# Performance work log

Hardware: AMD Instinct MI355X
Metric: run time of the kernel (lower is better)

## Reference

```python
import jax, jax.numpy as jnp
import numpy as np

STAGE = 100
EPS = 1e-5


def bin_affine(w, shift_aff, sign_aff):
    """Vectorized equivalent of the 100-iteration range-mask loop.
    Original: for i in range(stage): mask = (w >= lo_i) & (w < hi_i);
              shift += w.detach()*shift_aff[i]*mask; sign += w.detach()*sign_aff[i]*mask.
    Equivalent to bucketize + gather + scale. Element equal to w.max() falls
    outside every half-open bin (strict <), so it gets zero, matching torch.
    w is detached in the original, so gradients flow only to the affines.
    """
    wf = w.reshape(-1)
    wmin, wmax = wf.min(), wf.max()
    t = (wf - wmin) / (wmax - wmin) * STAGE
    idx = jnp.floor(t).astype(jnp.int32)
    valid = (idx >= 0) & (idx < STAGE)
    idxc = jnp.clip(idx, 0, STAGE - 1)
    wd = jax.lax.stop_gradient(wf)
    shift = jnp.where(valid, wd * shift_aff[idxc], 0.0)
    sign = jnp.where(valid, wd * sign_aff[idxc], 0.0)
    return shift.reshape(w.shape), sign.reshape(w.shape)


def eff_weight(w, shift_aff, sign_aff):
    # Conv2dShift forward with externally-assigned continuous shift/sign:
    # effective weight = sign * 2**shift (deepshift-style, unrounded).
    shift, sign = bin_affine(w, shift_aff, sign_aff)
    return sign * jnp.exp2(shift)


def conv2d(x, w, stride=1, pad=0, groups=1):
    return jax.lax.conv_general_dilated(
        x, w, (stride, stride), [(pad, pad), (pad, pad)],
        dimension_numbers=("NCHW", "OIHW", "NCHW"), feature_group_count=groups)


def batchnorm(x, g, b):
    m = x.mean((0, 2, 3), keepdims=True)
    v = x.var((0, 2, 3), keepdims=True)
    return (x - m) * jax.lax.rsqrt(v + EPS) * g[None, :, None, None] + b[None, :, None, None]


def setup_inputs() -> dict:
    key = jax.random.key(0)
    ks = jax.random.split(key, 16)
    d = {
        "x": jax.random.normal(ks[0], (32, 256, 56, 56), jnp.float32),
        "w_ds": 0.05 * jax.random.normal(ks[1], (512, 256, 1, 1), jnp.float32),
        "w_c1": 0.05 * jax.random.normal(ks[2], (128, 256, 1, 1), jnp.float32),
        "w_peg": 0.05 * jax.random.normal(ks[3], (128, 1, 3, 3), jnp.float32),
        "w_c2": 0.05 * jax.random.normal(ks[4], (128, 128, 3, 3), jnp.float32),
        "w_c3": 0.05 * jax.random.normal(ks[5], (512, 128, 1, 1), jnp.float32),
        "aff_ds_shift": jax.random.normal(ks[6], (STAGE,), jnp.float32),
        "aff_ds_sign": jax.random.normal(ks[7], (STAGE,), jnp.float32),
        "aff_c1_shift": jax.random.normal(ks[8], (STAGE,), jnp.float32),
        "aff_c1_sign": jax.random.normal(ks[9], (STAGE,), jnp.float32),
        "aff_c2_shift": jax.random.normal(ks[10], (STAGE,), jnp.float32),
        "aff_c2_sign": jax.random.normal(ks[11], (STAGE,), jnp.float32),
        "aff_c3_shift": jax.random.normal(ks[12], (STAGE,), jnp.float32),
        "aff_c3_sign": jax.random.normal(ks[13], (STAGE,), jnp.float32),
        "g_bn_ds": jnp.ones((512,), jnp.float32),
        "b_bn_ds": jnp.zeros((512,), jnp.float32),
        "g_bn1": jnp.ones((128,), jnp.float32),
        "b_bn1": jnp.zeros((128,), jnp.float32),
        "g_bn2": jnp.ones((128,), jnp.float32),
        "b_bn2": jnp.zeros((128,), jnp.float32),
        "g_bn3": jnp.ones((512,), jnp.float32),
        "b_bn3": jnp.zeros((512,), jnp.float32),
    }
    return d


def reference(x, w_ds, w_c1, w_peg, w_c2, w_c3,
              aff_ds_shift, aff_ds_sign, aff_c1_shift, aff_c1_sign,
              aff_c2_shift, aff_c2_sign, aff_c3_shift, aff_c3_sign,
              g_bn_ds, b_bn_ds, g_bn1, b_bn1, g_bn2, b_bn2, g_bn3, b_bn3):
    # main branch (fmap_size == self.fmap_size): bin downsample + conv1/2/3 weights
    wds_e = eff_weight(w_ds, aff_ds_shift, aff_ds_sign)
    wc1_e = eff_weight(w_c1, aff_c1_shift, aff_c1_sign)
    wc2_e = eff_weight(w_c2, aff_c2_shift, aff_c2_sign)
    wc3_e = eff_weight(w_c3, aff_c3_shift, aff_c3_sign)

    # downsample = Conv1x1 -> BN -> ReLU
    residual = jax.nn.relu(batchnorm(conv2d(x, wds_e), g_bn_ds, b_bn_ds))

    h = conv2d(x, wc1_e)                                   # 1x1, 256->128
    h = conv2d(h, w_peg, stride=1, pad=1, groups=128)      # PEG depthwise 3x3
    h = jax.nn.relu(batchnorm(h, g_bn1, b_bn1))            # bn1 + act1
    h = conv2d(h, wc2_e, stride=1, pad=1)                  # 3x3, 128->128
    h = jax.nn.relu(batchnorm(h, g_bn2, b_bn2))            # bn2 + act2
    h = conv2d(h, wc3_e)                                   # 1x1, 128->512
    h = batchnorm(h, g_bn3, b_bn3)                         # bn3
    return jax.nn.relu(h + residual)                       # act3
```

## Files before the change

kernel.cpp:

```cpp
#include <hip/hip_runtime.h>
#include <stdint.h>


#define HW    3136
#define WID   56
#define NB    32
#define FLIP_TENSOR 1

#define OFF_MM    0
#define OFF_SC1   8
#define OFF_BI1   136
#define OFF_SC2   264
#define OFF_BI2   392
#define OFF_SC3   520
#define OFF_BI3   1032
#define OFF_SCDS  1544
#define OFF_BIDS  2056
#define WB_BASE_BYTES 16384ULL
#define WB_M  0ULL
#define WB_C2 163840ULL
#define WB_C3 311296ULL
#define PS1S_B  786432ULL
#define PS1Q_B  802816ULL
#define PS2S_B  819200ULL
#define PS2Q_B  1622016ULL
#define PS3S_B  2424832ULL
#define PS3Q_B  5636096ULL
#define PSDS_B  8847360ULL
#define PSDQ_B  12058624ULL
#define AC_BASE_BYTES 16777216ULL
#define AC_A 0ULL
#define AC_B 12845056ULL
#define AC_C 25690112ULL
#define AC_R 77070336ULL
#define NSLOT 1568

typedef __attribute__((ext_vector_type(8))) short bfrag8;
typedef __attribute__((ext_vector_type(4))) float facc4;

__device__ __forceinline__ unsigned short f2bf(float f) {
  unsigned u = __float_as_uint(f);
  u = u + 0x7FFFu + ((u >> 16) & 1u);
  return (unsigned short)(u >> 16);
}
__device__ __forceinline__ float bf2f(unsigned short h) {
  return __uint_as_float(((unsigned)h) << 16);
}
__device__ __forceinline__ unsigned fmap(float f) {
  unsigned u = __float_as_uint(f);
  return (u & 0x80000000u) ? ~u : (u | 0x80000000u);
}
__device__ __forceinline__ float funmap(unsigned m) {
  unsigned u = (m & 0x80000000u) ? (m & 0x7FFFFFFFu) : ~m;
  return __uint_as_float(u);
}

__global__ void k_mm_init(unsigned* mm) {
  int t = threadIdx.x;
  if (t < 4) { mm[2 * t] = 0xFFFFFFFFu; mm[2 * t + 1] = 0u; }
}

__device__ __forceinline__ void tensor_of(int g0, int& tensor, int& local0) {
  if (g0 < 131072)      { tensor = 0; local0 = g0; }
  else if (g0 < 163840) { tensor = 1; local0 = g0 - 131072; }
  else if (g0 < 311296) { tensor = 2; local0 = g0 - 163840; }
  else                  { tensor = 3; local0 = g0 - 311296; }
}

__global__ __launch_bounds__(256) void k_minmax(
    const float* __restrict__ w_ds, const float* __restrict__ w_c1,
    const float* __restrict__ w_c2, const float* __restrict__ w_c3,
    unsigned* __restrict__ mm) {
  __shared__ unsigned smin[256], smax[256];
  int t = threadIdx.x;
  int tensor, local0;
  tensor_of(blockIdx.x * 1024, tensor, local0);
  const float* src = (tensor == 0) ? w_ds : (tensor == 1) ? w_c1 : (tensor == 2) ? w_c2 : w_c3;
  float4 v = *(const float4*)(src + local0 + t * 4);
  unsigned mn, mx;
  {
    unsigned m0 = fmap(v.x), m1 = fmap(v.y), m2 = fmap(v.z), m3 = fmap(v.w);
    mn = min(min(m0, m1), min(m2, m3));
    mx = max(max(m0, m1), max(m2, m3));
  }
  smin[t] = mn; smax[t] = mx;
  __syncthreads();
  for (int s = 128; s > 0; s >>= 1) {
    if (t < s) { smin[t] = min(smin[t], smin[t + s]); smax[t] = max(smax[t], smax[t + s]); }
    __syncthreads();
  }
  if (t == 0) {
    atomicMin(&mm[2 * tensor], smin[0]);
    atomicMax(&mm[2 * tensor + 1], smax[0]);
  }
}

__global__ __launch_bounds__(256) void k_effw(
    const float* __restrict__ w_ds, const float* __restrict__ w_c1,
    const float* __restrict__ w_c2, const float* __restrict__ w_c3,
    const float* __restrict__ sh_ds, const float* __restrict__ sg_ds,
    const float* __restrict__ sh_c1, const float* __restrict__ sg_c1,
    const float* __restrict__ sh_c2, const float* __restrict__ sg_c2,
    const float* __restrict__ sh_c3, const float* __restrict__ sg_c3,
    const unsigned* __restrict__ mm, unsigned short* __restrict__ wb) {
  int t = threadIdx.x;
  int tensor, local0;
  tensor_of(blockIdx.x * 1024, tensor, local0);
  const float* src = (tensor == 0) ? w_ds : (tensor == 1) ? w_c1 : (tensor == 2) ? w_c2 : w_c3;
  const float* sha = (tensor == 0) ? sh_ds : (tensor == 1) ? sh_c1 : (tensor == 2) ? sh_c2 : sh_c3;
  const float* sga = (tensor == 0) ? sg_ds : (tensor == 1) ? sg_c1 : (tensor == 2) ? sg_c2 : sg_c3;
  float wmin = funmap(mm[2 * tensor]);
  float wmax = funmap(mm[2 * tensor + 1]);
  float rng = __fsub_rn(wmax, wmin);
  float I32 = __fdiv_rn(rng, 100.0f);
  float edge100 = __fadd_rn(wmin, __fmul_rn(100.0f, I32));
  bool s32 = (wmax < edge100);
  bool binmax = (tensor == FLIP_TENSOR) ? !s32 : s32;
  float4 v4 = *(const float4*)(src + local0 + t * 4);
  float vs[4] = {v4.x, v4.y, v4.z, v4.w};
#pragma unroll
  for (int e = 0; e < 4; ++e) {
    int l = local0 + t * 4 + e;
    float v = vs[e];
    float ew;
    if (v == wmax) {
      ew = binmax ? (v * sga[99]) * exp2f(v * sha[99]) : 0.0f;
    } else {
      float tt = __fmul_rn(__fdiv_rn(__fsub_rn(v, wmin), rng), 100.0f);
      int idx = (int)floorf(tt);
      bool valid = (idx >= 0) && (idx < 100);
      int ic = valid ? idx : 0;
      float shift = valid ? v * sha[ic] : 0.0f;
      float sign  = valid ? v * sga[ic] : 0.0f;
      ew = sign * exp2f(shift);
    }
    unsigned short h = f2bf(ew);
    if (tensor == 0) {
      int co = l >> 8, ci = l & 255;
      wb[WB_M + (size_t)(128 + co) * 256 + ci] = h;
    } else if (tensor == 1) {
      int co = l >> 8, ci = l & 255;
      wb[WB_M + (size_t)co * 256 + ci] = h;
    } else if (tensor == 2) {
      int co = l / 1152; int r2 = l - co * 1152;
      int ci = r2 / 9; int tap = r2 - ci * 9;
      wb[WB_C2 + (size_t)co * 1152 + tap * 128 + ci] = h;
    } else {
      int co = l >> 7, ci = l & 127;
      wb[WB_C3 + (size_t)co * 128 + ci] = h;
    }
  }
}

template <int CI, int TAPS, int KBLK, int COOUT, bool XBF,
          bool FUSEIN, bool STATS, bool MERGED, int NCOB>
__global__ __launch_bounds__(256) void k_mconv6(
    const void* __restrict__ Xv, const unsigned short* __restrict__ Wt,
    unsigned short* __restrict__ Y1, unsigned short* __restrict__ Y2,
    const float* __restrict__ fsc, const float* __restrict__ fbi,
    float* __restrict__ PS, float* __restrict__ PQ) {
  constexpr int NSP = (TAPS == 9) ? 192 : 64;
  constexpr int ST  = KBLK + 2;
  __shared__ short lx[NSP][ST];
  __shared__ float redS[128][2], redQ[128][2];
  const int tid  = threadIdx.x;
  const int lane = tid & 63;
  const int wv   = tid >> 6;
  int lid = blockIdx.x;
  int xcd = lid & 7;
  int j   = lid >> 3;
  int co_blk = j % NCOB;
  int t_  = xcd * 196 + j / NCOB;
  int sp_blk = t_ % 49;
  int n      = t_ / 49;
  const int s0  = sp_blk * 64;
  const int co0 = co_blk * 128;
  const int NK  = CI * TAPS;
  const unsigned short* Xh = (const unsigned short*)Xv + (size_t)n * CI * HW;
  const float*          Xf = (const float*)Xv + (size_t)n * CI * HW;

  const int wco  = (wv >> 1) * 64;
  const int wsp  = (wv & 1) * 32;
  const int lrow = lane & 15;
  const int lkg  = lane >> 4;
  const int kb8  = lkg * 8;

  int spl[2], yc[2], xc[2];
#pragma unroll
  for (int nn = 0; nn < 2; ++nn) {
    spl[nn] = wsp + nn * 16 + lrow;
    int s = s0 + spl[nn];
    yc[nn] = s / WID;
    xc[nn] = s - yc[nn] * WID;
  }

  facc4 acc[4][2];
#pragma unroll
  for (int m = 0; m < 4; ++m)
#pragma unroll
    for (int nn = 0; nn < 2; ++nn) acc[m][nn] = (facc4)(0.0f);

  for (int k0 = 0; k0 < CI; k0 += KBLK) {
    __syncthreads();
    if (TAPS == 9) {
#pragma unroll
      for (int i = 0; i < 3; ++i) {
        int task = tid + i * 256;
        int spi = task % 192;
        int kc  = task / 192;
        int p = s0 - 64 + spi;
        short v[8];
        if ((unsigned)p < (unsigned)HW) {
          const unsigned short* pp = Xh + (size_t)(k0 + kc * 8) * HW + p;
#pragma unroll
          for (int jj = 0; jj < 8; ++jj) {
            if (FUSEIN) {
              float f = bf2f(pp[(size_t)jj * HW]);
              f = fmaxf(fmaf(f, fsc[k0 + kc * 8 + jj], fbi[k0 + kc * 8 + jj]), 0.0f);
              v[jj] = (short)f2bf(f);
            } else {
              v[jj] = (short)pp[(size_t)jj * HW];
            }
          }
        } else {
#pragma unroll
          for (int jj = 0; jj < 8; ++jj) v[jj] = 0;
        }
        *(short4*)(&lx[spi][kc * 8])     = (short4){v[0], v[1], v[2], v[3]};
        *(short4*)(&lx[spi][kc * 8 + 4]) = (short4){v[4], v[5], v[6], v[7]};
      }
    } else {
#pragma unroll
      for (int i = 0; i < KBLK / 32; ++i) {
        int task = tid + i * 256;
        int spi = task & 63;
        int kc  = task >> 6;
        int p = s0 + spi;
        short v[8];
        if (XBF) {
          const unsigned short* pp = Xh + (size_t)(k0 + kc * 8) * HW + p;
#pragma unroll
          for (int jj = 0; jj < 8; ++jj) {
            if (FUSEIN) {
              float f = bf2f(pp[(size_t)jj * HW]);
              f = fmaxf(fmaf(f, fsc[k0 + kc * 8 + jj], fbi[k0 + kc * 8 + jj]), 0.0f);
              v[jj] = (short)f2bf(f);
            } else {
              v[jj] = (short)pp[(size_t)jj * HW];
            }
          }
        } else {
          const float* pf = Xf + (size_t)(k0 + kc * 8) * HW + p;
#pragma unroll
          for (int jj = 0; jj < 8; ++jj) v[jj] = (short)f2bf(pf[(size_t)jj * HW]);
        }
        *(short4*)(&lx[spi][kc * 8])     = (short4){v[0], v[1], v[2], v[3]};
        *(short4*)(&lx[spi][kc * 8 + 4]) = (short4){v[4], v[5], v[6], v[7]};
      }
    }
    __syncthreads();
    if (TAPS == 1) {
      bfrag8 af[KBLK / 32][4];
#pragma unroll
      for (int kk = 0; kk < KBLK / 32; ++kk)
#pragma unroll
        for (int m = 0; m < 4; ++m)
          af[kk][m] = *(const bfrag8*)(Wt +
              (size_t)(co0 + wco + m * 16 + lrow) * NK + k0 + kk * 32 + kb8);
#pragma unroll
      for (int kk = 0; kk < KBLK / 32; ++kk) {
#pragma unroll
        for (int nn = 0; nn < 2; ++nn) {
          bfrag8 b = *(const bfrag8*)(&lx[spl[nn]][kk * 32 + kb8]);
#pragma unroll
          for (int m = 0; m < 4; ++m)
            acc[m][nn] = __builtin_amdgcn_mfma_f32_16x16x32_bf16(
                af[kk][m], b, acc[m][nn], 0, 0, 0);
        }
      }
    } else {
      bfrag8 afc[4], afn[4];
#pragma unroll
      for (int m = 0; m < 4; ++m)
        afc[m] = *(const bfrag8*)(Wt +
            (size_t)(co0 + wco + m * 16 + lrow) * NK + k0 + kb8);
      for (int tap = 0; tap < 9; ++tap) {
        if (tap < 8) {
#pragma unroll
          for (int m = 0; m < 4; ++m)
            afn[m] = *(const bfrag8*)(Wt +
                (size_t)(co0 + wco + m * 16 + lrow) * NK + (tap + 1) * CI + k0 + kb8);
        }
        const int dy = tap / 3 - 1;
        const int dx = tap % 3 - 1;
        const int off = dy * WID + dx;
#pragma unroll
        for (int nn = 0; nn < 2; ++nn) {
          bfrag8 b = *(const bfrag8*)(&lx[64 + spl[nn] + off][kb8]);
          bool valid = ((unsigned)(xc[nn] + dx) < (unsigned)WID) &&
                       ((unsigned)(yc[nn] + dy) < (unsigned)WID);
          if (!valid) b = (bfrag8)(short)0;
#pragma unroll
          for (int m = 0; m < 4; ++m)
            acc[m][nn] = __builtin_amdgcn_mfma_f32_16x16x32_bf16(
                afc[m], b, acc[m][nn], 0, 0, 0);
        }
#pragma unroll
        for (int m = 0; m < 4; ++m) afc[m] = afn[m];
      }
    }
  }
  unsigned short* Yb;
  int coL, COst;
  if (MERGED) {
    if (co0 < 128) { Yb = Y1; coL = co0; COst = 128; }
    else           { Yb = Y2; coL = co0 - 128; COst = 512; }
  } else {
    Yb = Y1; coL = co0; COst = COOUT;
  }
#pragma unroll
  for (int m = 0; m < 4; ++m)
#pragma unroll
    for (int nn = 0; nn < 2; ++nn)
#pragma unroll
      for (int r = 0; r < 4; ++r) {
        int co_g = coL + wco + m * 16 + lkg * 4 + r;
        int sp_g = s0 + wsp + nn * 16 + lrow;
        Yb[((size_t)n * COst + co_g) * HW + sp_g] = f2bf(acc[m][nn][r]);
      }
  const bool do_st = STATS && (!MERGED || co0 >= 128);
  if (do_st) {
#pragma unroll
    for (int m = 0; m < 4; ++m)
#pragma unroll
      for (int r = 0; r < 4; ++r) {
        float sv = acc[m][0][r] + acc[m][1][r];
        float qv = acc[m][0][r] * acc[m][0][r] + acc[m][1][r] * acc[m][1][r];
#pragma unroll
        for (int d = 1; d < 16; d <<= 1) {
          sv += __shfl_xor(sv, d);
          qv += __shfl_xor(qv, d);
        }
        if (lrow == 0) {
          int col = wco + m * 16 + lkg * 4 + r;
          redS[col][wv & 1] = sv;
          redQ[col][wv & 1] = qv;
        }
      }
    __syncthreads();
    if (tid < 128) {
      int cstat = (MERGED ? co0 - 128 : co0) + tid;
      int slot = n * 49 + sp_blk;
      PS[(size_t)cstat * NSLOT + slot] = redS[tid][0] + redS[tid][1];
      PQ[(size_t)cstat * NSLOT + slot] = redQ[tid][0] + redQ[tid][1];
    }
  }
}

__global__ __launch_bounds__(256) void k_dw(
    const unsigned short* __restrict__ Xin, const float* __restrict__ wp,
    unsigned short* __restrict__ Yout,
    float* __restrict__ PS, float* __restrict__ PQ) {
  __shared__ float pl[HW];
  __shared__ float rs[256], rq[256];
  int bid = blockIdx.x;
  int c = bid & 127;
  int n = bid >> 7;
  const unsigned short* src = Xin + (size_t)bid * HW;
  int t = threadIdx.x;
  for (int q = t; q < HW / 4; q += 256) {
    ushort4 h4 = *(const ushort4*)(src + q * 4);
    pl[q * 4 + 0] = bf2f(h4.x); pl[q * 4 + 1] = bf2f(h4.y);
    pl[q * 4 + 2] = bf2f(h4.z); pl[q * 4 + 3] = bf2f(h4.w);
  }
  float w[9];
#pragma unroll
  for (int k = 0; k < 9; ++k) w[k] = wp[c * 9 + k];
  __syncthreads();
  unsigned short* dst = Yout + (size_t)bid * HW;
  float accS = 0.0f, accQ = 0.0f;
  for (int q = t; q < HW / 4; q += 256) {
    float o[4];
#pragma unroll
    for (int e = 0; e < 4; ++e) {
      int s = q * 4 + e;
      int y = s / WID, xcc = s - y * WID;
      float accv = 0.0f;
#pragma unroll
      for (int ky = 0; ky < 3; ++ky) {
        int yy = y + ky - 1;
        if (yy < 0 || yy >= WID) continue;
#pragma unroll
        for (int kx = 0; kx < 3; ++kx) {
          int xx = xcc + kx - 1;
          if (xx < 0 || xx >= WID) continue;
          accv = fmaf(w[ky * 3 + kx], pl[yy * WID + xx], accv);
        }
      }
      o[e] = accv;
      accS += accv;
      accQ = fmaf(accv, accv, accQ);
    }
    ushort4 ov;
    ov.x = f2bf(o[0]); ov.y = f2bf(o[1]); ov.z = f2bf(o[2]); ov.w = f2bf(o[3]);
    *(ushort4*)(dst + q * 4) = ov;
  }
  rs[t] = accS; rq[t] = accQ;
  __syncthreads();
  for (int st = 128; st > 0; st >>= 1) {
    if (t < st) { rs[t] += rs[t + st]; rq[t] += rq[t + st]; }
    __syncthreads();
  }
  if (t == 0) {
    PS[(size_t)c * NB + n] = rs[0];
    PQ[(size_t)c * NB + n] = rq[0];
  }
}

__global__ __launch_bounds__(256) void k_red(
    const float* __restrict__ S, const float* __restrict__ Q,
    const float* __restrict__ g, const float* __restrict__ b,
    float* __restrict__ sc_o, float* __restrict__ bi_o, int npart) {
  int c = blockIdx.x, t = threadIdx.x;
  double s = 0.0, q = 0.0;
  for (int i = t; i < npart; i += 256) {
    s += S[(size_t)c * npart + i];
    q += Q[(size_t)c * npart + i];
  }
  __shared__ double ss[256], qq[256];
  ss[t] = s; qq[t] = q;
  __syncthreads();
  for (int st = 128; st > 0; st >>= 1) {
    if (t < st) { ss[t] += ss[t + st]; qq[t] += qq[t + st]; }
    __syncthreads();
  }
  if (t == 0) {
    double nn = (double)HW * NB;
    double mean = ss[0] / nn;
    double var = qq[0] / nn - mean * mean;
    float rstd = (float)(1.0 / sqrt(var + 1e-5));
    float sc = g[c] * rstd;
    sc_o[c] = sc;
    bi_o[c] = b[c] - (float)mean * sc;
  }
}

__global__ __launch_bounds__(256) void k_final(
    float* __restrict__ out, const unsigned short* __restrict__ hC,
    const unsigned short* __restrict__ r,
    const float* __restrict__ sc3, const float* __restrict__ bi3,
    const float* __restrict__ scds, const float* __restrict__ bids) {
  const int QPN = 512 * 784;
  const int total = NB * QPN;
  for (int q = blockIdx.x * 256 + threadIdx.x; q < total; q += gridDim.x * 256) {
    int qn = q % QPN;
    int c = qn / 784;
    ushort4 hh = *(const ushort4*)(hC + (size_t)q * 4);
    ushort4 rh = *(const ushort4*)(r + (size_t)q * 4);
    float s3 = sc3[c], b3 = bi3[c], sd = scds[c], bd = bids[c];
    float4 o;
    float rb;
    rb = fmaxf(fmaf(bf2f(rh.x), sd, bd), 0.0f); o.x = fmaxf(fmaf(bf2f(hh.x), s3, b3) + rb, 0.0f);
    rb = fmaxf(fmaf(bf2f(rh.y), sd, bd), 0.0f); o.y = fmaxf(fmaf(bf2f(hh.y), s3, b3) + rb, 0.0f);
    rb = fmaxf(fmaf(bf2f(rh.z), sd, bd), 0.0f); o.z = fmaxf(fmaf(bf2f(hh.z), s3, b3) + rb, 0.0f);
    rb = fmaxf(fmaf(bf2f(rh.w), sd, bd), 0.0f); o.w = fmaxf(fmaf(bf2f(hh.w), s3, b3) + rb, 0.0f);
    *(float4*)(out + (size_t)q * 4) = o;
  }
}

extern "C" void kernel_launch(void* const* d_in, const int* in_sizes, int n_in,
                              void* d_out, int out_size, void* d_ws, size_t ws_size,
                              hipStream_t stream) {
  const float *x = nullptr, *w_ds = nullptr, *w_c1 = nullptr, *w_peg = nullptr,
              *w_c2 = nullptr, *w_c3 = nullptr;
  const float* aff[8] = {nullptr};
  const float* v512[4] = {nullptr};
  const float* v128[4] = {nullptr};
  int naff = 0, n512 = 0, n128 = 0;
  for (int i = 0; i < n_in; ++i) {
    const float* p = (const float*)d_in[i];
    switch (in_sizes[i]) {
      case 25690112: x = p; break;
      case 131072:   w_ds = p; break;
      case 32768:    w_c1 = p; break;
      case 1152:     w_peg = p; break;
      case 147456:   w_c2 = p; break;
      case 65536:    w_c3 = p; break;
      case 100:      if (naff < 8) aff[naff++] = p; break;
      case 512:      if (n512 < 4) v512[n512++] = p; break;
      case 128:      if (n128 < 4) v128[n128++] = p; break;
      default: break;
    }
  }
  const float *a_ds_sh = aff[0], *a_ds_sg = aff[1], *a_c1_sh = aff[2], *a_c1_sg = aff[3];
  const float *a_c2_sh = aff[4], *a_c2_sg = aff[5], *a_c3_sh = aff[6], *a_c3_sg = aff[7];
  const float *g_ds = v512[0], *b_ds = v512[1], *g3 = v512[2], *b3 = v512[3];
  const float *g1 = v128[0], *b1 = v128[1], *g2 = v128[2], *b2 = v128[3];

  float* ws  = (float*)d_ws;
  float* out = (float*)d_out;
  unsigned* mm = (unsigned*)(ws + OFF_MM);
  unsigned short* wb = (unsigned short*)((char*)d_ws + WB_BASE_BYTES);
  unsigned short* ac = (unsigned short*)((char*)d_ws + AC_BASE_BYTES);
  unsigned short* bufA = ac + AC_A;
  unsigned short* bufB = ac + AC_B;
  unsigned short* bufC = ac + AC_C;
  unsigned short* bufR = ac + AC_R;
  float* ps1S = (float*)((char*)d_ws + PS1S_B);
  float* ps1Q = (float*)((char*)d_ws + PS1Q_B);
  float* ps2S = (float*)((char*)d_ws + PS2S_B);
  float* ps2Q = (float*)((char*)d_ws + PS2Q_B);
  float* ps3S = (float*)((char*)d_ws + PS3S_B);
  float* ps3Q = (float*)((char*)d_ws + PS3Q_B);
  float* psdS = (float*)((char*)d_ws + PSDS_B);
  float* psdQ = (float*)((char*)d_ws + PSDQ_B);

  k_mm_init<<<dim3(1), dim3(64), 0, stream>>>(mm);
  k_minmax<<<dim3(368), dim3(256), 0, stream>>>(w_ds, w_c1, w_c2, w_c3, mm);
  k_effw<<<dim3(368), dim3(256), 0, stream>>>(
      w_ds, w_c1, w_c2, w_c3,
      a_ds_sh, a_ds_sg, a_c1_sh, a_c1_sg, a_c2_sh, a_c2_sg, a_c3_sh, a_c3_sg,
      mm, wb);

  k_mconv6<256, 1, 128, 0, false, false, true, true, 5>
      <<<dim3(7840), dim3(256), 0, stream>>>(
      x, wb + WB_M, bufA, bufR, nullptr, nullptr, psdS, psdQ);
  k_red<<<dim3(512), dim3(256), 0, stream>>>(psdS, psdQ, g_ds, b_ds,
                                             ws + OFF_SCDS, ws + OFF_BIDS, NSLOT);
  k_dw<<<dim3(NB * 128), dim3(256), 0, stream>>>(bufA, w_peg, bufB, ps1S, ps1Q);
  k_red<<<dim3(128), dim3(256), 0, stream>>>(ps1S, ps1Q, g1, b1,
                                             ws + OFF_SC1, ws + OFF_BI1, NB);
  k_mconv6<128, 9, 32, 128, true, true, true, false, 1>
      <<<dim3(1568), dim3(256), 0, stream>>>(
      bufB, wb + WB_C2, bufA, nullptr, ws + OFF_SC1, ws + OFF_BI1, ps2S, ps2Q);
  k_red<<<dim3(128), dim3(256), 0, stream>>>(ps2S, ps2Q, g2, b2,
                                             ws + OFF_SC2, ws + OFF_BI2, NSLOT);
  k_mconv6<128, 1, 128, 512, true, true, true, false, 4>
      <<<dim3(6272), dim3(256), 0, stream>>>(
      bufA, wb + WB_C3, bufC, nullptr, ws + OFF_SC2, ws + OFF_BI2, ps3S, ps3Q);
  k_red<<<dim3(512), dim3(256), 0, stream>>>(ps3S, ps3Q, g3, b3,
                                             ws + OFF_SC3, ws + OFF_BI3, NSLOT);
  k_final<<<dim3(4096), dim3(256), 0, stream>>>(out, bufC, bufR,
                                                ws + OFF_SC3, ws + OFF_BI3,
                                                ws + OFF_SCDS, ws + OFF_BIDS);
}
```

Before: 545.4 us.

## Switch intermediate activations to channels-last layout with input transpose kernel

Adds a transpose kernel that converts x to bf16 NHWC, and switches the conv and depthwise kernels to read and write channels-last intermediates with 16-byte vector loads instead of strided per-channel gathers. The depthwise kernel is re-tiled over spatial blocks with per-slot BN statistics. The final conv writes fp32 directly into the output buffer, and the epilogue then updates it in place, which drops the bf16 intermediate buffer. In exchange it adds an extra pass over x and moves more fp32 traffic through the last conv.

```diff
diff --git a/kernel.cpp b/kernel.cpp
--- a/kernel.cpp
+++ b/kernel.cpp
@@ -21,18 +21,18 @@
 #define WB_C2 163840ULL
 #define WB_C3 311296ULL
 #define PS1S_B  786432ULL
-#define PS1Q_B  802816ULL
-#define PS2S_B  819200ULL
-#define PS2Q_B  1622016ULL
-#define PS3S_B  2424832ULL
-#define PS3Q_B  5636096ULL
-#define PSDS_B  8847360ULL
-#define PSDQ_B  12058624ULL
-#define AC_BASE_BYTES 16777216ULL
-#define AC_A 0ULL
-#define AC_B 12845056ULL
-#define AC_C 25690112ULL
-#define AC_R 77070336ULL
+#define PS1Q_B  1589248ULL
+#define PS2S_B  2392064ULL
+#define PS2Q_B  3194880ULL
+#define PS3S_B  3997696ULL
+#define PS3Q_B  7208960ULL
+#define PSDS_B  10420224ULL
+#define PSDQ_B  13631488ULL
+#define AC_BASE_BYTES 33554432ULL
+#define AC_XT 0ULL
+#define AC_A  25690112ULL
+#define AC_B  38535168ULL
+#define AC_R  51380224ULL
 #define NSLOT 1568
 
 typedef __attribute__((ext_vector_type(8))) short bfrag8;
@@ -152,16 +152,45 @@
   }
 }
 
-template <int CI, int TAPS, int KBLK, int COOUT, bool XBF,
-          bool FUSEIN, bool STATS, bool MERGED, int NCOB>
-__global__ __launch_bounds__(256) void k_mconv6(
-    const void* __restrict__ Xv, const unsigned short* __restrict__ Wt,
+__global__ __launch_bounds__(256) void k_tr(
+    const float* __restrict__ x, unsigned short* __restrict__ XT) {
+  __shared__ short lt[64 * 258];
+  int bid = blockIdx.x;
+  int sp_blk = bid % 49, n = bid / 49;
+  int s0 = sp_blk * 64;
+  int t = threadIdx.x;
+  {
+    const float* row = x + ((size_t)n * 256 + t) * HW + s0;
+#pragma unroll
+    for (int i = 0; i < 16; ++i) {
+      float4 v = *(const float4*)(row + i * 4);
+      lt[(i * 4 + 0) * 258 + t] = (short)f2bf(v.x);
+      lt[(i * 4 + 1) * 258 + t] = (short)f2bf(v.y);
+      lt[(i * 4 + 2) * 258 + t] = (short)f2bf(v.z);
+      lt[(i * 4 + 3) * 258 + t] = (short)f2bf(v.w);
+    }
+  }
+  __syncthreads();
+  {
+    int spi = t >> 2, cb = (t & 3) * 64;
+    unsigned short* dst = XT + ((size_t)n * HW + s0 + spi) * 256 + cb;
+    const short* srcl = &lt[spi * 258 + cb];
+#pragma unroll
+    for (int q = 0; q < 8; ++q)
+      *(float4*)((short*)dst + q * 8) = *(const float4*)(srcl + q * 8);
+  }
+}
+
+template <int CIN, int TAPS, int KBLK, int NCOB, bool FUSEIN, bool STATS, int MODE>
+__global__ __launch_bounds__(256) void k_mconv7(
+    const unsigned short* __restrict__ Xn, const unsigned short* __restrict__ Wt,
     unsigned short* __restrict__ Y1, unsigned short* __restrict__ Y2,
+    float* __restrict__ Yf,
     const float* __restrict__ fsc, const float* __restrict__ fbi,
     float* __restrict__ PS, float* __restrict__ PQ) {
   constexpr int NSP = (TAPS == 9) ? 192 : 64;
   constexpr int ST  = KBLK + 2;
-  __shared__ short lx[NSP][ST];
+  __shared__ short lx[NSP * ST];
   __shared__ float redS[128][2], redQ[128][2];
   const int tid  = threadIdx.x;
   const int lane = tid & 63;
@@ -175,9 +204,8 @@
   int n      = t_ / 49;
   const int s0  = sp_blk * 64;
   const int co0 = co_blk * 128;
-  const int NK  = CI * TAPS;
-  const unsigned short* Xh = (const unsigned short*)Xv + (size_t)n * CI * HW;
-  const float*          Xf = (const float*)Xv + (size_t)n * CI * HW;
+  const int NK  = CIN * TAPS;
+  const size_t nsp0 = (size_t)n * HW + s0;
 
   const int wco  = (wv >> 1) * 64;
   const int wsp  = (wv & 1) * 32;
@@ -200,62 +228,51 @@
 #pragma unroll
     for (int nn = 0; nn < 2; ++nn) acc[m][nn] = (facc4)(0.0f);
 
-  for (int k0 = 0; k0 < CI; k0 += KBLK) {
+  for (int k0 = 0; k0 < CIN; k0 += KBLK) {
     __syncthreads();
     if (TAPS == 9) {
 #pragma unroll
       for (int i = 0; i < 3; ++i) {
         int task = tid + i * 256;
-        int spi = task % 192;
-        int kc  = task / 192;
+        int spi = task >> 2, ch = (task & 3) * 8;
         int p = s0 - 64 + spi;
-        short v[8];
+        unsigned short vv[8];
         if ((unsigned)p < (unsigned)HW) {
-          const unsigned short* pp = Xh + (size_t)(k0 + kc * 8) * HW + p;
-#pragma unroll
-          for (int jj = 0; jj < 8; ++jj) {
+          float4 raw = *(const float4*)(Xn + ((size_t)n * HW + p) * CIN + k0 + ch);
+          const unsigned short* pv = (const unsigned short*)&raw;
+#pragma unroll
+          for (int q = 0; q < 8; ++q) {
             if (FUSEIN) {
-              float f = bf2f(pp[(size_t)jj * HW]);
-              f = fmaxf(fmaf(f, fsc[k0 + kc * 8 + jj], fbi[k0 + kc * 8 + jj]), 0.0f);
-              v[jj] = (short)f2bf(f);
-            } else {
-              v[jj] = (short)pp[(size_t)jj * HW];
-            }
+              float f = bf2f(pv[q]);
+              f = fmaxf(fmaf(f, fsc[k0 + ch + q], fbi[k0 + ch + q]), 0.0f);
+              vv[q] = f2bf(f);
+            } else vv[q] = pv[q];
           }
         } else {
 #pragma unroll
-          for (int jj = 0; jj < 8; ++jj) v[jj] = 0;
-        }
-        *(short4*)(&lx[spi][kc * 8])     = (short4){v[0], v[1], v[2], v[3]};
-        *(short4*)(&lx[spi][kc * 8 + 4]) = (short4){v[4], v[5], v[6], v[7]};
+          for (int q = 0; q < 8; ++q) vv[q] = 0;
+        }
+        *(float4*)(&lx[spi * ST + ch]) = *(const float4*)vv;
       }
     } else {
-#pragma unroll
-      for (int i = 0; i < KBLK / 32; ++i) {
-        int task = tid + i * 256;
-        int spi = task & 63;
-        int kc  = task >> 6;
-        int p = s0 + spi;
-        short v[8];
-        if (XBF) {
-          const unsigned short* pp = Xh + (size_t)(k0 + kc * 8) * HW + p;
-#pragma unroll
-          for (int jj = 0; jj < 8; ++jj) {
-            if (FUSEIN) {
-              float f = bf2f(pp[(size_t)jj * HW]);
-              f = fmaxf(fmaf(f, fsc[k0 + kc * 8 + jj], fbi[k0 + kc * 8 + jj]), 0.0f);
-              v[jj] = (short)f2bf(f);
-            } else {
-              v[jj] = (short)pp[(size_t)jj * HW];
-            }
+      int row = tid >> 2, cb = (tid & 3) * 32;
+      const unsigned short* src = Xn + (nsp0 + row) * CIN + k0 + cb;
+#pragma unroll
+      for (int q = 0; q < 4; ++q) {
+        float4 raw = *(const float4*)(src + q * 8);
+        if (FUSEIN) {
+          const unsigned short* pv = (const unsigned short*)&raw;
+          unsigned short vv[8];
+#pragma unroll
+          for (int e = 0; e < 8; ++e) {
+            float f = bf2f(pv[e]);
+            f = fmaxf(fmaf(f, fsc[k0 + cb + q * 8 + e], fbi[k0 + cb + q * 8 + e]), 0.0f);
+            vv[e] = f2bf(f);
           }
+          *(float4*)(&lx[row * ST + cb + q * 8]) = *(const float4*)vv;
         } else {
-          const float* pf = Xf + (size_t)(k0 + kc * 8) * HW + p;
-#pragma unroll
-          for (int jj = 0; jj < 8; ++jj) v[jj] = (short)f2bf(pf[(size_t)jj * HW]);
-        }
-        *(short4*)(&lx[spi][kc * 8])     = (short4){v[0], v[1], v[2], v[3]};
-        *(short4*)(&lx[spi][kc * 8 + 4]) = (short4){v[4], v[5], v[6], v[7]};
+          *(float4*)(&lx[row * ST + cb + q * 8]) = raw;
+        }
       }
     }
     __syncthreads();
@@ -271,7 +288,7 @@
       for (int kk = 0; kk < KBLK / 32; ++kk) {
 #pragma unroll
         for (int nn = 0; nn < 2; ++nn) {
-          bfrag8 b = *(const bfrag8*)(&lx[spl[nn]][kk * 32 + kb8]);
+          bfrag8 b = *(const bfrag8*)(&lx[spl[nn] * ST + kk * 32 + kb8]);
 #pragma unroll
           for (int m = 0; m < 4; ++m)
             acc[m][nn] = __builtin_amdgcn_mfma_f32_16x16x32_bf16(
@@ -289,14 +306,14 @@
 #pragma unroll
           for (int m = 0; m < 4; ++m)
             afn[m] = *(const bfrag8*)(Wt +
-                (size_t)(co0 + wco + m * 16 + lrow) * NK + (tap + 1) * CI + k0 + kb8);
+                (size_t)(co0 + wco + m * 16 + lrow) * NK + (tap + 1) * CIN + k0 + kb8);
         }
         const int dy = tap / 3 - 1;
         const int dx = tap % 3 - 1;
         const int off = dy * WID + dx;
 #pragma unroll
         for (int nn = 0; nn < 2; ++nn) {
-          bfrag8 b = *(const bfrag8*)(&lx[64 + spl[nn] + off][kb8]);
+          bfrag8 b = *(const bfrag8*)(&lx[(64 + spl[nn] + off) * ST + kb8]);
           bool valid = ((unsigned)(xc[nn] + dx) < (unsigned)WID) &&
                        ((unsigned)(yc[nn] + dy) < (unsigned)WID);
           if (!valid) b = (bfrag8)(short)0;
@@ -310,25 +327,40 @@
       }
     }
   }
-  unsigned short* Yb;
-  int coL, COst;
-  if (MERGED) {
-    if (co0 < 128) { Yb = Y1; coL = co0; COst = 128; }
-    else           { Yb = Y2; coL = co0 - 128; COst = 512; }
+  if (MODE == 0 || (MODE == 2 && co0 < 128)) {
+#pragma unroll
+    for (int m = 0; m < 4; ++m)
+#pragma unroll
+      for (int nn = 0; nn < 2; ++nn) {
+        unsigned short o[4];
+#pragma unroll
+        for (int r = 0; r < 4; ++r) o[r] = f2bf(acc[m][nn][r]);
+        size_t addr = (nsp0 + spl[nn]) * 128 + co0 + wco + m * 16 + lkg * 4;
+        *(ushort4*)(Y1 + addr) = *(const ushort4*)o;
+      }
+  } else if (MODE == 2) {
+    int coL = co0 - 128;
+#pragma unroll
+    for (int m = 0; m < 4; ++m)
+#pragma unroll
+      for (int nn = 0; nn < 2; ++nn)
+#pragma unroll
+        for (int r = 0; r < 4; ++r) {
+          int co_g = coL + wco + m * 16 + lkg * 4 + r;
+          Y2[((size_t)n * 512 + co_g) * HW + s0 + spl[nn]] = f2bf(acc[m][nn][r]);
+        }
   } else {
-    Yb = Y1; coL = co0; COst = COOUT;
-  }
-#pragma unroll
-  for (int m = 0; m < 4; ++m)
-#pragma unroll
-    for (int nn = 0; nn < 2; ++nn)
-#pragma unroll
-      for (int r = 0; r < 4; ++r) {
-        int co_g = coL + wco + m * 16 + lkg * 4 + r;
-        int sp_g = s0 + wsp + nn * 16 + lrow;
-        Yb[((size_t)n * COst + co_g) * HW + sp_g] = f2bf(acc[m][nn][r]);
-      }
-  const bool do_st = STATS && (!MERGED || co0 >= 128);
+#pragma unroll
+    for (int m = 0; m < 4; ++m)
+#pragma unroll
+      for (int nn = 0; nn < 2; ++nn)
+#pragma unroll
+        for (int r = 0; r < 4; ++r) {
+          int co_g = co0 + wco + m * 16 + lkg * 4 + r;
+          Yf[((size_t)n * 512 + co_g) * HW + s0 + spl[nn]] = acc[m][nn][r];
+        }
+  }
+  const bool do_st = STATS && (MODE != 2 || co0 >= 128);
   if (do_st) {
 #pragma unroll
     for (int m = 0; m < 4; ++m)
@@ -349,7 +381,7 @@
       }
     __syncthreads();
     if (tid < 128) {
-      int cstat = (MERGED ? co0 - 128 : co0) + tid;
+      int cstat = ((MODE == 2) ? co0 - 128 : co0) + tid;
       int slot = n * 49 + sp_blk;
       PS[(size_t)cstat * NSLOT + slot] = redS[tid][0] + redS[tid][1];
       PQ[(size_t)cstat * NSLOT + slot] = redQ[tid][0] + redQ[tid][1];
@@ -358,62 +390,68 @@
 }
 
 __global__ __launch_bounds__(256) void k_dw(
-    const unsigned short* __restrict__ Xin, const float* __restrict__ wp,
-    unsigned short* __restrict__ Yout,
+    const unsigned short* __restrict__ Ain, const float* __restrict__ wp,
+    unsigned short* __restrict__ Bout,
     float* __restrict__ PS, float* __restrict__ PQ) {
-  __shared__ float pl[HW];
-  __shared__ float rs[256], rq[256];
+  __shared__ float wl[9][128];
+  __shared__ float sS[16][128], sQ[16][128];
   int bid = blockIdx.x;
-  int c = bid & 127;
-  int n = bid >> 7;
-  const unsigned short* src = Xin + (size_t)bid * HW;
+  int sp_blk = bid % 49, n = bid / 49;
+  int s0 = sp_blk * 64;
   int t = threadIdx.x;
-  for (int q = t; q < HW / 4; q += 256) {
-    ushort4 h4 = *(const ushort4*)(src + q * 4);
-    pl[q * 4 + 0] = bf2f(h4.x); pl[q * 4 + 1] = bf2f(h4.y);
-    pl[q * 4 + 2] = bf2f(h4.z); pl[q * 4 + 3] = bf2f(h4.w);
-  }
-  float w[9];
-#pragma unroll
-  for (int k = 0; k < 9; ++k) w[k] = wp[c * 9 + k];
+  if (t < 128) {
+#pragma unroll
+    for (int tap = 0; tap < 9; ++tap) wl[tap][t] = wp[t * 9 + tap];
+  }
   __syncthreads();
-  unsigned short* dst = Yout + (size_t)bid * HW;
-  float accS = 0.0f, accQ = 0.0f;
-  for (int q = t; q < HW / 4; q += 256) {
-    float o[4];
-#pragma unroll
-    for (int e = 0; e < 4; ++e) {
-      int s = q * 4 + e;
-      int y = s / WID, xcc = s - y * WID;
-      float accv = 0.0f;
-#pragma unroll
-      for (int ky = 0; ky < 3; ++ky) {
-        int yy = y + ky - 1;
-        if (yy < 0 || yy >= WID) continue;
-#pragma unroll
-        for (int kx = 0; kx < 3; ++kx) {
-          int xx = xcc + kx - 1;
-          if (xx < 0 || xx >= WID) continue;
-          accv = fmaf(w[ky * 3 + kx], pl[yy * WID + xx], accv);
-        }
-      }
-      o[e] = accv;
-      accS += accv;
-      accQ = fmaf(accv, accv, accQ);
-    }
-    ushort4 ov;
-    ov.x = f2bf(o[0]); ov.y = f2bf(o[1]); ov.z = f2bf(o[2]); ov.w = f2bf(o[3]);
-    *(ushort4*)(dst + q * 4) = ov;
-  }
-  rs[t] = accS; rq[t] = accQ;
+  const int c8 = (t & 15) * 8;
+  const int g  = t >> 4;
+  float wreg[9][8];
+#pragma unroll
+  for (int tap = 0; tap < 9; ++tap)
+#pragma unroll
+    for (int jj = 0; jj < 8; ++jj) wreg[tap][jj] = wl[tap][c8 + jj];
+  float aS[8], aQ[8];
+#pragma unroll
+  for (int jj = 0; jj < 8; ++jj) { aS[jj] = 0.0f; aQ[jj] = 0.0f; }
+  const size_t nb = (size_t)n * HW;
+#pragma unroll
+  for (int it = 0; it < 4; ++it) {
+    int s = s0 + it * 16 + g;
+    int y = s / WID, xx0 = s - y * WID;
+    float accv[8];
+#pragma unroll
+    for (int jj = 0; jj < 8; ++jj) accv[jj] = 0.0f;
+#pragma unroll
+    for (int tap = 0; tap < 9; ++tap) {
+      int dy = tap / 3 - 1, dx = tap % 3 - 1;
+      if ((unsigned)(y + dy) < (unsigned)WID && (unsigned)(xx0 + dx) < (unsigned)WID) {
+        float4 raw = *(const float4*)(Ain + (nb + s + dy * WID + dx) * 128 + c8);
+        const unsigned short* pv = (const unsigned short*)&raw;
+#pragma unroll
+        for (int jj = 0; jj < 8; ++jj)
+          accv[jj] = fmaf(wreg[tap][jj], bf2f(pv[jj]), accv[jj]);
+      }
+    }
+    unsigned short ov[8];
+#pragma unroll
+    for (int jj = 0; jj < 8; ++jj) {
+      ov[jj] = f2bf(accv[jj]);
+      aS[jj] += accv[jj];
+      aQ[jj] = fmaf(accv[jj], accv[jj], aQ[jj]);
+    }
+    *(float4*)(Bout + (nb + s) * 128 + c8) = *(const float4*)ov;
+  }
+#pragma unroll
+  for (int jj = 0; jj < 8; ++jj) { sS[g][c8 + jj] = aS[jj]; sQ[g][c8 + jj] = aQ[jj]; }
   __syncthreads();
-  for (int st = 128; st > 0; st >>= 1) {
-    if (t < st) { rs[t] += rs[t + st]; rq[t] += rq[t + st]; }
-    __syncthreads();
-  }
-  if (t == 0) {
-    PS[(size_t)c * NB + n] = rs[0];
-    PQ[(size_t)c * NB + n] = rq[0];
+  if (t < 128) {
+    float s = 0.0f, q = 0.0f;
+#pragma unroll
+    for (int g2 = 0; g2 < 16; ++g2) { s += sS[g2][t]; q += sQ[g2][t]; }
+    int slot = n * 49 + sp_blk;
+    PS[(size_t)t * NSLOT + slot] = s;
+    PQ[(size_t)t * NSLOT + slot] = q;
   }
 }
 
@@ -446,8 +484,7 @@
 }
 
 __global__ __launch_bounds__(256) void k_final(
-    float* __restrict__ out, const unsigned short* __restrict__ hC,
-    const unsigned short* __restrict__ r,
+    float* __restrict__ out, const unsigned short* __restrict__ r,
     const float* __restrict__ sc3, const float* __restrict__ bi3,
     const float* __restrict__ scds, const float* __restrict__ bids) {
   const int QPN = 512 * 784;
@@ -455,15 +492,15 @@
   for (int q = blockIdx.x * 256 + threadIdx.x; q < total; q += gridDim.x * 256) {
     int qn = q % QPN;
     int c = qn / 784;
-    ushort4 hh = *(const ushort4*)(hC + (size_t)q * 4);
+    float4 h = *(const float4*)(out + (size_t)q * 4);
     ushort4 rh = *(const ushort4*)(r + (size_t)q * 4);
     float s3 = sc3[c], b3 = bi3[c], sd = scds[c], bd = bids[c];
     float4 o;
     float rb;
-    rb = fmaxf(fmaf(bf2f(rh.x), sd, bd), 0.0f); o.x = fmaxf(fmaf(bf2f(hh.x), s3, b3) + rb, 0.0f);
-    rb = fmaxf(fmaf(bf2f(rh.y), sd, bd), 0.0f); o.y = fmaxf(fmaf(bf2f(hh.y), s3, b3) + rb, 0.0f);
-    rb = fmaxf(fmaf(bf2f(rh.z), sd, bd), 0.0f); o.z = fmaxf(fmaf(bf2f(hh.z), s3, b3) + rb, 0.0f);
-    rb = fmaxf(fmaf(bf2f(rh.w), sd, bd), 0.0f); o.w = fmaxf(fmaf(bf2f(hh.w), s3, b3) + rb, 0.0f);
+    rb = fmaxf(fmaf(bf2f(rh.x), sd, bd), 0.0f); o.x = fmaxf(fmaf(h.x, s3, b3) + rb, 0.0f);
+    rb = fmaxf(fmaf(bf2f(rh.y), sd, bd), 0.0f); o.y = fmaxf(fmaf(h.y, s3, b3) + rb, 0.0f);
+    rb = fmaxf(fmaf(bf2f(rh.z), sd, bd), 0.0f); o.z = fmaxf(fmaf(h.z, s3, b3) + rb, 0.0f);
+    rb = fmaxf(fmaf(bf2f(rh.w), sd, bd), 0.0f); o.w = fmaxf(fmaf(h.w, s3, b3) + rb, 0.0f);
     *(float4*)(out + (size_t)q * 4) = o;
   }
 }
@@ -502,10 +539,10 @@
   unsigned* mm = (unsigned*)(ws + OFF_MM);
   unsigned short* wb = (unsigned short*)((char*)d_ws + WB_BASE_BYTES);
   unsigned short* ac = (unsigned short*)((char*)d_ws + AC_BASE_BYTES);
-  unsigned short* bufA = ac + AC_A;
-  unsigned short* bufB = ac + AC_B;
-  unsigned short* bufC = ac + AC_C;
-  unsigned short* bufR = ac + AC_R;
+  unsigned short* bufXT = ac + AC_XT;
+  unsigned short* bufA  = ac + AC_A;
+  unsigned short* bufB  = ac + AC_B;
+  unsigned short* bufR  = ac + AC_R;
   float* ps1S = (float*)((char*)d_ws + PS1S_B);
   float* ps1Q = (float*)((char*)d_ws + PS1Q_B);
   float* ps2S = (float*)((char*)d_ws + PS2S_B);
@@ -521,26 +558,29 @@
       w_ds, w_c1, w_c2, w_c3,
       a_ds_sh, a_ds_sg, a_c1_sh, a_c1_sg, a_c2_sh, a_c2_sg, a_c3_sh, a_c3_sg,
       mm, wb);
-
-  k_mconv6<256, 1, 128, 0, false, false, true, true, 5>
+  k_tr<<<dim3(1568), dim3(256), 0, stream>>>(x, bufXT);
+
+  k_mconv7<256, 1, 128, 5, false, true, 2>
       <<<dim3(7840), dim3(256), 0, stream>>>(
-      x, wb + WB_M, bufA, bufR, nullptr, nullptr, psdS, psdQ);
+      bufXT, wb + WB_M, bufA, bufR, nullptr, nullptr, nullptr, psdS, psdQ);
   k_red<<<dim3(512), dim3(256), 0, stream>>>(psdS, psdQ, g_ds, b_ds,
                                              ws + OFF_SCDS, ws + OFF_BIDS, NSLOT);
-  k_dw<<<dim3(NB * 128), dim3(256), 0, stream>>>(bufA, w_peg, bufB, ps1S, ps1Q);
+  k_dw<<<dim3(1568), dim3(256), 0, stream>>>(bufA, w_peg, bufB, ps1S, ps1Q);
   k_red<<<dim3(128), dim3(256), 0, stream>>>(ps1S, ps1Q, g1, b1,
-                                             ws + OFF_SC1, ws + OFF_BI1, NB);
-  k_mconv6<128, 9, 32, 128, true, true, true, false, 1>
+                                             ws + OFF_SC1, ws + OFF_BI1, NSLOT);
+  k_mconv7<128, 9, 32, 1, true, true, 0>
       <<<dim3(1568), dim3(256), 0, stream>>>(
-      bufB, wb + WB_C2, bufA, nullptr, ws + OFF_SC1, ws + OFF_BI1, ps2S, ps2Q);
+      bufB, wb + WB_C2, bufA, nullptr, nullptr, ws + OFF_SC1, ws + OFF_BI1,
+      ps2S, ps2Q);
   k_red<<<dim3(128), dim3(256), 0, stream>>>(ps2S, ps2Q, g2, b2,
                                              ws + OFF_SC2, ws + OFF_BI2, NSLOT);
-  k_mconv6<128, 1, 128, 512, true, true, true, false, 4>
+  k_mconv7<128, 1, 128, 4, true, true, 3>
       <<<dim3(6272), dim3(256), 0, stream>>>(
-      bufA, wb + WB_C3, bufC, nullptr, ws + OFF_SC2, ws + OFF_BI2, ps3S, ps3Q);
+      bufA, wb + WB_C3, nullptr, nullptr, out, ws + OFF_SC2, ws + OFF_BI2,
+      ps3S, ps3Q);
   k_red<<<dim3(512), dim3(256), 0, stream>>>(ps3S, ps3Q, g3, b3,
                                              ws + OFF_SC3, ws + OFF_BI3, NSLOT);
-  k_final<<<dim3(4096), dim3(256), 0, stream>>>(out, bufC, bufR,
+  k_final<<<dim3(4096), dim3(256), 0, stream>>>(out, bufR,
                                                 ws + OFF_SC3, ws + OFF_BI3,
                                                 ws + OFF_SCDS, ws + OFF_BIDS);
 }
```

New measurement: 601.1 us. 1.1x slower.

## Pre-transpose input to bf16 NHWC and use LDS-direct loads for merged 1x1 conv

Applied to the files above, without the earlier changes.

Adds a transpose kernel that converts the fp32 NCHW input into a bf16 spatial-major (channels-last) buffer. A new specialized merged conv1/downsample kernel then stages this buffer straight into LDS with global_load_lds and an XOR swizzle to avoid bank conflicts. The aim is to cut the fp32 read and in-kernel conversion and transpose cost that the five channel-block passes over x previously repeated. The extra pass writes and re-reads a bf16 copy of x, and that copy reuses buffer C, which is only safe because conv3 writes C later.

```diff
diff --git a/kernel.cpp b/kernel.cpp
--- a/kernel.cpp
+++ b/kernel.cpp
@@ -33,6 +33,7 @@
 #define AC_B 12845056ULL
 #define AC_C 25690112ULL
 #define AC_R 77070336ULL
+#define AC_XT AC_C
 #define NSLOT 1568
 
 typedef __attribute__((ext_vector_type(8))) short bfrag8;
@@ -53,6 +54,13 @@
 __device__ __forceinline__ float funmap(unsigned m) {
   unsigned u = (m & 0x80000000u) ? (m & 0x7FFFFFFFu) : ~m;
   return __uint_as_float(u);
+}
+
+__device__ __forceinline__ void gload_lds16(const void* g, void* l) {
+  __builtin_amdgcn_global_load_lds(
+      (const __attribute__((address_space(1))) unsigned int*)g,
+      (__attribute__((address_space(3))) unsigned int*)l,
+      16, 0, 0);
 }
 
 __global__ void k_mm_init(unsigned* mm) {
@@ -152,11 +160,155 @@
   }
 }
 
+__global__ __launch_bounds__(256) void k_tr(
+    const float* __restrict__ x, unsigned short* __restrict__ XT) {
+  __shared__ short lt[64 * 258];
+  int bid = blockIdx.x;
+  int sp_blk = bid % 49, n = bid / 49;
+  int s0 = sp_blk * 64;
+  int t = threadIdx.x;
+  {
+    const float* row = x + ((size_t)n * 256 + t) * HW + s0;
+#pragma unroll
+    for (int i = 0; i < 16; ++i) {
+      float4 v = *(const float4*)(row + i * 4);
+      lt[(i * 4 + 0) * 258 + t] = (short)f2bf(v.x);
+      lt[(i * 4 + 1) * 258 + t] = (short)f2bf(v.y);
+      lt[(i * 4 + 2) * 258 + t] = (short)f2bf(v.z);
+      lt[(i * 4 + 3) * 258 + t] = (short)f2bf(v.w);
+    }
+  }
+  __syncthreads();
+  {
+    int spi = t >> 2, cb = (t & 3) * 64;
+    unsigned short* dst = XT + ((size_t)n * HW + s0 + spi) * 256 + cb;
+    const short* srcl = &lt[spi * 258 + cb];
+#pragma unroll
+    for (int q = 0; q < 8; ++q)
+      *(float4*)((short*)dst + q * 8) = *(const float4*)(srcl + q * 8);
+  }
+}
+
+__global__ __launch_bounds__(256) void k_mconvG(
+    const unsigned short* __restrict__ XT, const unsigned short* __restrict__ Wt,
+    unsigned short* __restrict__ Y1, unsigned short* __restrict__ Y2,
+    float* __restrict__ PS, float* __restrict__ PQ) {
+  __shared__ short lx[64 * 128];
+  __shared__ float redS[128][2], redQ[128][2];
+  const int tid  = threadIdx.x;
+  const int lane = tid & 63;
+  const int wv   = tid >> 6;
+  int lid = blockIdx.x;
+  int xcd = lid & 7;
+  int j   = lid >> 3;
+  int co_blk = j % 5;
+  int t_  = xcd * 196 + j / 5;
+  int sp_blk = t_ % 49;
+  int n      = t_ / 49;
+  const int s0  = sp_blk * 64;
+  const int co0 = co_blk * 128;
+  const size_t nsp0 = (size_t)n * HW + s0;
+
+  const int wco  = (wv >> 1) * 64;
+  const int wsp  = (wv & 1) * 32;
+  const int lrow = lane & 15;
+  const int lkg  = lane >> 4;
+  const int kb8  = lkg * 8;
+
+  int spl[2];
+#pragma unroll
+  for (int nn = 0; nn < 2; ++nn) spl[nn] = wsp + nn * 16 + lrow;
+
+  facc4 acc[4][2];
+#pragma unroll
+  for (int m = 0; m < 4; ++m)
+#pragma unroll
+    for (int nn = 0; nn < 2; ++nn) acc[m][nn] = (facc4)(0.0f);
+
+#pragma unroll
+  for (int ph = 0; ph < 2; ++ph) {
+    const int k0 = ph * 128;
+    __syncthreads();
+#pragma unroll
+    for (int i = 0; i < 4; ++i) {
+      int B  = tid * 16 + i * 4096;
+      int sp = B >> 8;
+      int p  = (B >> 4) & 15;
+      int c  = p ^ (sp & 7);
+      const unsigned short* g = XT + (nsp0 + sp) * 256 + k0 + c * 8;
+      gload_lds16(g, (char*)lx + B);
+    }
+    __syncthreads();
+    bfrag8 af[4][4];
+#pragma unroll
+    for (int kk = 0; kk < 4; ++kk)
+#pragma unroll
+      for (int m = 0; m < 4; ++m)
+        af[kk][m] = *(const bfrag8*)(Wt +
+            (size_t)(co0 + wco + m * 16 + lrow) * 256 + k0 + kk * 32 + kb8);
+#pragma unroll
+    for (int kk = 0; kk < 4; ++kk) {
+#pragma unroll
+      for (int nn = 0; nn < 2; ++nn) {
+        int row = spl[nn];
+        int chunk = (kk * 4 + lkg) ^ (row & 7);
+        bfrag8 b = *(const bfrag8*)((const char*)lx + row * 256 + (chunk << 4));
+#pragma unroll
+        for (int m = 0; m < 4; ++m)
+          acc[m][nn] = __builtin_amdgcn_mfma_f32_16x16x32_bf16(
+              af[kk][m], b, acc[m][nn], 0, 0, 0);
+      }
+    }
+  }
+  {
+    unsigned short* Yb;
+    int coL, COst;
+    if (co0 < 128) { Yb = Y1; coL = co0; COst = 128; }
+    else           { Yb = Y2; coL = co0 - 128; COst = 512; }
+#pragma unroll
+    for (int m = 0; m < 4; ++m)
+#pragma unroll
+      for (int nn = 0; nn < 2; ++nn)
+#pragma unroll
+        for (int r = 0; r < 4; ++r) {
+          int co_g = coL + wco + m * 16 + lkg * 4 + r;
+          int sp_g = s0 + wsp + nn * 16 + lrow;
+          Yb[((size_t)n * COst + co_g) * HW + sp_g] = f2bf(acc[m][nn][r]);
+        }
+  }
+  if (co0 >= 128) {
+#pragma unroll
+    for (int m = 0; m < 4; ++m)
+#pragma unroll
+      for (int r = 0; r < 4; ++r) {
+        float sv = acc[m][0][r] + acc[m][1][r];
+        float qv = acc[m][0][r] * acc[m][0][r] + acc[m][1][r] * acc[m][1][r];
+#pragma unroll
+        for (int d = 1; d < 16; d <<= 1) {
+          sv += __shfl_xor(sv, d);
+          qv += __shfl_xor(qv, d);
+        }
+        if (lrow == 0) {
+          int col = wco + m * 16 + lkg * 4 + r;
+          redS[col][wv & 1] = sv;
+          redQ[col][wv & 1] = qv;
+        }
+      }
+    __syncthreads();
+    if (tid < 128) {
+      int cstat = co0 - 128 + tid;
+      int slot = n * 49 + sp_blk;
+      PS[(size_t)cstat * NSLOT + slot] = redS[tid][0] + redS[tid][1];
+      PQ[(size_t)cstat * NSLOT + slot] = redQ[tid][0] + redQ[tid][1];
+    }
+  }
+}
+
 template <int CI, int TAPS, int KBLK, int COOUT, bool XBF,
-          bool FUSEIN, bool STATS, bool MERGED, int NCOB>
+          bool FUSEIN, bool STATS, int NCOB>
 __global__ __launch_bounds__(256) void k_mconv6(
     const void* __restrict__ Xv, const unsigned short* __restrict__ Wt,
-    unsigned short* __restrict__ Y1, unsigned short* __restrict__ Y2,
+    unsigned short* __restrict__ Y1,
     const float* __restrict__ fsc, const float* __restrict__ fbi,
     float* __restrict__ PS, float* __restrict__ PQ) {
   constexpr int NSP = (TAPS == 9) ? 192 : 64;
@@ -310,26 +462,17 @@
       }
     }
   }
-  unsigned short* Yb;
-  int coL, COst;
-  if (MERGED) {
-    if (co0 < 128) { Yb = Y1; coL = co0; COst = 128; }
-    else           { Yb = Y2; coL = co0 - 128; COst = 512; }
-  } else {
-    Yb = Y1; coL = co0; COst = COOUT;
-  }
 #pragma unroll
   for (int m = 0; m < 4; ++m)
 #pragma unroll
     for (int nn = 0; nn < 2; ++nn)
 #pragma unroll
       for (int r = 0; r < 4; ++r) {
-        int co_g = coL + wco + m * 16 + lkg * 4 + r;
+        int co_g = co0 + wco + m * 16 + lkg * 4 + r;
         int sp_g = s0 + wsp + nn * 16 + lrow;
-        Yb[((size_t)n * COst + co_g) * HW + sp_g] = f2bf(acc[m][nn][r]);
-      }
-  const bool do_st = STATS && (!MERGED || co0 >= 128);
-  if (do_st) {
+        Y1[((size_t)n * COOUT + co_g) * HW + sp_g] = f2bf(acc[m][nn][r]);
+      }
+  if (STATS) {
 #pragma unroll
     for (int m = 0; m < 4; ++m)
 #pragma unroll
@@ -349,7 +492,7 @@
       }
     __syncthreads();
     if (tid < 128) {
-      int cstat = (MERGED ? co0 - 128 : co0) + tid;
+      int cstat = co0 + tid;
       int slot = n * 49 + sp_blk;
       PS[(size_t)cstat * NSLOT + slot] = redS[tid][0] + redS[tid][1];
       PQ[(size_t)cstat * NSLOT + slot] = redQ[tid][0] + redQ[tid][1];
@@ -502,10 +645,11 @@
   unsigned* mm = (unsigned*)(ws + OFF_MM);
   unsigned short* wb = (unsigned short*)((char*)d_ws + WB_BASE_BYTES);
   unsigned short* ac = (unsigned short*)((char*)d_ws + AC_BASE_BYTES);
-  unsigned short* bufA = ac + AC_A;
-  unsigned short* bufB = ac + AC_B;
-  unsigned short* bufC = ac + AC_C;
-  unsigned short* bufR = ac + AC_R;
+  unsigned short* bufA  = ac + AC_A;
+  unsigned short* bufB  = ac + AC_B;
+  unsigned short* bufC  = ac + AC_C;
+  unsigned short* bufR  = ac + AC_R;
+  unsigned short* bufXT = ac + AC_XT;
   float* ps1S = (float*)((char*)d_ws + PS1S_B);
   float* ps1Q = (float*)((char*)d_ws + PS1Q_B);
   float* ps2S = (float*)((char*)d_ws + PS2S_B);
@@ -521,23 +665,23 @@
       w_ds, w_c1, w_c2, w_c3,
       a_ds_sh, a_ds_sg, a_c1_sh, a_c1_sg, a_c2_sh, a_c2_sg, a_c3_sh, a_c3_sg,
       mm, wb);
-
-  k_mconv6<256, 1, 128, 0, false, false, true, true, 5>
-      <<<dim3(7840), dim3(256), 0, stream>>>(
-      x, wb + WB_M, bufA, bufR, nullptr, nullptr, psdS, psdQ);
+  k_tr<<<dim3(1568), dim3(256), 0, stream>>>(x, bufXT);
+
+  k_mconvG<<<dim3(7840), dim3(256), 0, stream>>>(
+      bufXT, wb + WB_M, bufA, bufR, psdS, psdQ);
   k_red<<<dim3(512), dim3(256), 0, stream>>>(psdS, psdQ, g_ds, b_ds,
                                              ws + OFF_SCDS, ws + OFF_BIDS, NSLOT);
   k_dw<<<dim3(NB * 128), dim3(256), 0, stream>>>(bufA, w_peg, bufB, ps1S, ps1Q);
   k_red<<<dim3(128), dim3(256), 0, stream>>>(ps1S, ps1Q, g1, b1,
                                              ws + OFF_SC1, ws + OFF_BI1, NB);
-  k_mconv6<128, 9, 32, 128, true, true, true, false, 1>
+  k_mconv6<128, 9, 32, 128, true, true, true, 1>
       <<<dim3(1568), dim3(256), 0, stream>>>(
-      bufB, wb + WB_C2, bufA, nullptr, ws + OFF_SC1, ws + OFF_BI1, ps2S, ps2Q);
+      bufB, wb + WB_C2, bufA, ws + OFF_SC1, ws + OFF_BI1, ps2S, ps2Q);
   k_red<<<dim3(128), dim3(256), 0, stream>>>(ps2S, ps2Q, g2, b2,
                                              ws + OFF_SC2, ws + OFF_BI2, NSLOT);
-  k_mconv6<128, 1, 128, 512, true, true, true, false, 4>
+  k_mconv6<128, 1, 128, 512, true, true, true, 4>
       <<<dim3(6272), dim3(256), 0, stream>>>(
-      bufA, wb + WB_C3, bufC, nullptr, ws + OFF_SC2, ws + OFF_BI2, ps3S, ps3Q);
+      bufA, wb + WB_C3, bufC, ws + OFF_SC2, ws + OFF_BI2, ps3S, ps3Q);
   k_red<<<dim3(512), dim3(256), 0, stream>>>(ps3S, ps3Q, g3, b3,
                                              ws + OFF_SC3, ws + OFF_BI3, NSLOT);
   k_final<<<dim3(4096), dim3(256), 0, stream>>>(out, bufC, bufR,
```

Result: no change. 554.3 us (+1.6%).
